# Kernel tuning notes

Hardware: AMD Instinct MI355X
Metric: run time of the kernel (lower is better)

Reference implementation:

```python
import jax, jax.numpy as jnp
import numpy as np

B, M, NH, EH = 16, 128, 256, 128


def setup_inputs() -> dict:
    key = jax.random.key(0)
    ks = jax.random.split(key, 10)
    s = 0.05
    return {
        "X": jax.random.normal(ks[0], (B, M, NH), dtype=jnp.float32),
        "E": jax.random.normal(ks[1], (B, M, M, EH), dtype=jnp.float32),
        "A": jax.random.uniform(ks[2], (B, M, M), dtype=jnp.float32),
        "w": jax.random.uniform(ks[3], (B, M, 1), dtype=jnp.float32),
        "Wv_w": jax.random.normal(ks[4], (NH, NH), dtype=jnp.float32) * s,
        "Wv_b": jnp.zeros((NH,), dtype=jnp.float32),
        "We_w": jax.random.normal(ks[5], (EH, EH), dtype=jnp.float32) * s,
        "We_b": jnp.zeros((EH,), dtype=jnp.float32),
        "Wu_w": jax.random.normal(ks[6], (2 * NH + EH, NH), dtype=jnp.float32) * s,
        "Wu_b": jnp.zeros((NH,), dtype=jnp.float32),
    }


def reference(X, E, A, w, Wv_w, Wv_b, We_w, We_b, Wu_w, Wu_b):
    act = jax.nn.relu
    # W_v / W_e single-layer FFNs (capacity=0 -> one Linear)
    node_map = X @ Wv_w + Wv_b                      # [B, m, nh]
    edge_map = E @ We_w + We_b                      # [B, m, m, eh]
    # Fused aggregation: sum_i A[b,i,j] * cat(node_map[b,i], edge_map[b,i,j])
    # (avoids materializing the [B,m,m,nh+eh] intermediate; same math)
    agg_node = jnp.einsum('bij,bid->bjd', A, node_map)   # [B, m, nh]
    agg_edge = jnp.einsum('bij,bije->bje', A, edge_map)  # [B, m, eh]
    h = jnp.concatenate([agg_node, agg_edge, X], axis=2) # [B, m, 2nh+eh]
    out = (act(h) @ Wu_w + Wu_b) * w                     # [B, m, nh]
    return out
```

## Files before the change

kernel.cpp:

```cpp
#include <hip/hip_runtime.h>

namespace {

constexpr int Bn   = 16;
constexpr int Mn   = 128;
constexpr int NHn  = 256;
constexpr int EHn  = 128;
constexpr int ROWS = Bn * Mn;
constexpr int HW   = 2 * NHn + EHn;

__device__ __forceinline__ float4 ld4(const float* p) {
    return *reinterpret_cast<const float4*>(p);
}
__device__ __forceinline__ float4 f4relu(const float4& a) {
    return make_float4(fmaxf(a.x, 0.f), fmaxf(a.y, 0.f),
                       fmaxf(a.z, 0.f), fmaxf(a.w, 0.f));
}

__global__ __launch_bounds__(256) void k_reduce(
    const float* __restrict__ E, const float* __restrict__ A,
    float* __restrict__ T)
{
    const int bid = blockIdx.x;
    const int b   = bid >> 5;
    const int j0  = (bid & 31) * 4;
    const int tid = threadIdx.x;

    __shared__ float acolT[4][Mn];

    if (tid < Mn) {
        const float4 a4 = ld4(A + (size_t)b * Mn * Mn + (size_t)tid * Mn + j0);
        acolT[0][tid] = a4.x; acolT[1][tid] = a4.y;
        acolT[2][tid] = a4.z; acolT[3][tid] = a4.w;
    }
    __syncthreads();

    const int jj = tid >> 6;
    const int f2 = tid & 63;
    const float* Eb = E + (size_t)b * Mn * Mn * EHn + (size_t)(j0 + jj) * EHn
                        + f2 * 2;
    const float* ac = acolT[jj];

    float2 acc = make_float2(0.f, 0.f);
    #pragma unroll 16
    for (int i = 0; i < Mn; ++i) {
        const float2 e2 = *reinterpret_cast<const float2*>(
            Eb + (size_t)i * (Mn * EHn));
        const float a = ac[i];
        acc.x = fmaf(a, e2.x, acc.x);
        acc.y = fmaf(a, e2.y, acc.y);
    }

    const int row = b * Mn + j0 + jj;
    *reinterpret_cast<float2*>(T + (size_t)row * EHn + f2 * 2) = acc;
}

__global__ __launch_bounds__(256) void k_mix(
    const float* __restrict__ T, const float* __restrict__ A,
    const float* __restrict__ X,
    const float* __restrict__ Wv, const float* __restrict__ Wvb,
    const float* __restrict__ We, const float* __restrict__ Web,
    const float* __restrict__ Wu, const float* __restrict__ Wub,
    const float* __restrict__ wrow, float* __restrict__ out)
{
    const int bid = blockIdx.x;
    const int b   = bid >> 5;
    const int j0  = (bid & 31) * 4;
    const int r0  = b * Mn + j0;
    const int tid = threadIdx.x;

    __shared__ float acolT[4][Mn];
    __shared__ float ts[4][EHn];
    __shared__ float axs[4][NHn];
    __shared__ float hs[4][HW];
    __shared__ float pec[2][4][EHn];
    __shared__ float pcs[4][16];
    __shared__ float csb[4];

    if (tid < Mn) {
        const float4 a4 = ld4(A + (size_t)b * Mn * Mn + (size_t)tid * Mn + j0);
        acolT[0][tid] = a4.x; acolT[1][tid] = a4.y;
        acolT[2][tid] = a4.z; acolT[3][tid] = a4.w;
    } else {
        const int t = tid - 128;
        const int r = t >> 5, c = t & 31;
        *reinterpret_cast<float4*>(&ts[r][c * 4]) =
            ld4(T + (size_t)(r0 + r) * EHn + c * 4);
    }
    {
        const int r = tid >> 6, c = tid & 63;
        const float4 x4 = ld4(X + (size_t)(r0 + r) * NHn + c * 4);
        *reinterpret_cast<float4*>(&hs[r][NHn + EHn + c * 4]) = f4relu(x4);
    }
    __syncthreads();

    if (tid < 64) {
        const int r = tid >> 4, s = tid & 15;
        float acc = 0.f;
        #pragma unroll
        for (int i = 0; i < 8; ++i) acc += acolT[r][s * 8 + i];
        pcs[r][s] = acc;
    }
    if (tid < 4) {
        float acc = 0.f;
        #pragma unroll
        for (int s = 0; s < 16; ++s) acc += pcs[tid][s];
        csb[tid] = acc;
    }

    {
        const float* Xb = X + (size_t)(b * Mn) * NHn + tid;
        float a0 = 0.f, a1 = 0.f, a2 = 0.f, a3 = 0.f;
        for (int k = 0; k < Mn; k += 16) {
            float xw[16];
            #pragma unroll
            for (int u = 0; u < 16; ++u) xw[u] = Xb[(size_t)(k + u) * NHn];
            #pragma unroll
            for (int u = 0; u < 16; ++u) {
                a0 = fmaf(acolT[0][k + u], xw[u], a0);
                a1 = fmaf(acolT[1][k + u], xw[u], a1);
                a2 = fmaf(acolT[2][k + u], xw[u], a2);
                a3 = fmaf(acolT[3][k + u], xw[u], a3);
            }
        }
        axs[0][tid] = a0; axs[1][tid] = a1;
        axs[2][tid] = a2; axs[3][tid] = a3;
    }
    __syncthreads();

    {
        const float* Wvc = Wv + tid;
        float n0 = 0.f, n1 = 0.f, n2 = 0.f, n3 = 0.f;
        for (int k = 0; k < NHn; k += 16) {
            float wv[16];
            #pragma unroll
            for (int u = 0; u < 16; ++u) wv[u] = Wvc[(size_t)(k + u) * NHn];
            #pragma unroll
            for (int u = 0; u < 16; ++u) {
                n0 = fmaf(axs[0][k + u], wv[u], n0);
                n1 = fmaf(axs[1][k + u], wv[u], n1);
                n2 = fmaf(axs[2][k + u], wv[u], n2);
                n3 = fmaf(axs[3][k + u], wv[u], n3);
            }
        }
        const float bv = Wvb[tid];
        hs[0][tid] = fmaxf(fmaf(csb[0], bv, n0), 0.f);
        hs[1][tid] = fmaxf(fmaf(csb[1], bv, n1), 0.f);
        hs[2][tid] = fmaxf(fmaf(csb[2], bv, n2), 0.f);
        hs[3][tid] = fmaxf(fmaf(csb[3], bv, n3), 0.f);
    }

    {
        const int kh = tid >> 7;
        const int c  = tid & 127;
        const int k0 = kh * 64;
        const float* Wec = We + c;
        float e0 = 0.f, e1 = 0.f, e2 = 0.f, e3 = 0.f;
        for (int k = k0; k < k0 + 64; k += 16) {
            float we[16];
            #pragma unroll
            for (int u = 0; u < 16; ++u) we[u] = Wec[(size_t)(k + u) * EHn];
            #pragma unroll
            for (int u = 0; u < 16; ++u) {
                e0 = fmaf(ts[0][k + u], we[u], e0);
                e1 = fmaf(ts[1][k + u], we[u], e1);
                e2 = fmaf(ts[2][k + u], we[u], e2);
                e3 = fmaf(ts[3][k + u], we[u], e3);
            }
        }
        pec[kh][0][c] = e0; pec[kh][1][c] = e1;
        pec[kh][2][c] = e2; pec[kh][3][c] = e3;
    }
    __syncthreads();
    if (tid < 128) {
        const float be = Web[tid];
        #pragma unroll
        for (int r = 0; r < 4; ++r) {
            const float e = pec[0][r][tid] + pec[1][r][tid];
            hs[r][NHn + tid] = fmaxf(fmaf(csb[r], be, e), 0.f);
        }
    }
    __syncthreads();

    {
        const float* Wuc = Wu + tid;
        float o0 = 0.f, o1 = 0.f, o2 = 0.f, o3 = 0.f;
        for (int k = 0; k < HW; k += 16) {
            float wu[16];
            #pragma unroll
            for (int u = 0; u < 16; ++u) wu[u] = Wuc[(size_t)(k + u) * NHn];
            #pragma unroll
            for (int u = 0; u < 16; ++u) {
                o0 = fmaf(hs[0][k + u], wu[u], o0);
                o1 = fmaf(hs[1][k + u], wu[u], o1);
                o2 = fmaf(hs[2][k + u], wu[u], o2);
                o3 = fmaf(hs[3][k + u], wu[u], o3);
            }
        }
        const float bu = Wub[tid];
        out[(size_t)(r0 + 0) * NHn + tid] = (o0 + bu) * wrow[r0 + 0];
        out[(size_t)(r0 + 1) * NHn + tid] = (o1 + bu) * wrow[r0 + 1];
        out[(size_t)(r0 + 2) * NHn + tid] = (o2 + bu) * wrow[r0 + 2];
        out[(size_t)(r0 + 3) * NHn + tid] = (o3 + bu) * wrow[r0 + 3];
    }
}

}

extern "C" void kernel_launch(void* const* d_in, const int* in_sizes, int n_in,
                              void* d_out, int out_size, void* d_ws, size_t ws_size,
                              hipStream_t stream) {
    const float* X   = (const float*)d_in[0];
    const float* E   = (const float*)d_in[1];
    const float* A   = (const float*)d_in[2];
    const float* w   = (const float*)d_in[3];
    const float* Wv  = (const float*)d_in[4];
    const float* Wvb = (const float*)d_in[5];
    const float* We  = (const float*)d_in[6];
    const float* Web = (const float*)d_in[7];
    const float* Wu  = (const float*)d_in[8];
    const float* Wub = (const float*)d_in[9];
    float* out = (float*)d_out;

    float* T = (float*)d_ws;

    k_reduce<<<512, 256, 0, stream>>>(E, A, T);
    k_mix<<<512, 256, 0, stream>>>(T, A, X, Wv, Wvb, We, Web, Wu, Wub, w, out);
}
```

Baseline: 258.8 us.

## Fuse edge reduction into mixing kernel and split i-range across thread halves

Merges the E·A reduction kernel into the mixing kernel, so the intermediate T buffer is never written to or read back from global memory and one launch is removed. Within the fused kernel, each thread reads float4 edge chunks and covers half of the i range, and the two partial sums are combined in shared memory. This adds an extra barrier and shared storage. Without a second kernel to overlap with, the memory-bound E stream now has to share each block with the matmul phases.

```diff
diff --git a/kernel.cpp b/kernel.cpp
--- a/kernel.cpp
+++ b/kernel.cpp
@@ -6,57 +6,24 @@
 constexpr int Mn   = 128;
 constexpr int NHn  = 256;
 constexpr int EHn  = 128;
-constexpr int ROWS = Bn * Mn;
 constexpr int HW   = 2 * NHn + EHn;
 
 __device__ __forceinline__ float4 ld4(const float* p) {
     return *reinterpret_cast<const float4*>(p);
+}
+__device__ __forceinline__ void f4fma(float4& acc, float a, const float4& v) {
+    acc.x = fmaf(a, v.x, acc.x);
+    acc.y = fmaf(a, v.y, acc.y);
+    acc.z = fmaf(a, v.z, acc.z);
+    acc.w = fmaf(a, v.w, acc.w);
 }
 __device__ __forceinline__ float4 f4relu(const float4& a) {
     return make_float4(fmaxf(a.x, 0.f), fmaxf(a.y, 0.f),
                        fmaxf(a.z, 0.f), fmaxf(a.w, 0.f));
 }
 
-__global__ __launch_bounds__(256) void k_reduce(
+__global__ __launch_bounds__(256) void k_fused(
     const float* __restrict__ E, const float* __restrict__ A,
-    float* __restrict__ T)
-{
-    const int bid = blockIdx.x;
-    const int b   = bid >> 5;
-    const int j0  = (bid & 31) * 4;
-    const int tid = threadIdx.x;
-
-    __shared__ float acolT[4][Mn];
-
-    if (tid < Mn) {
-        const float4 a4 = ld4(A + (size_t)b * Mn * Mn + (size_t)tid * Mn + j0);
-        acolT[0][tid] = a4.x; acolT[1][tid] = a4.y;
-        acolT[2][tid] = a4.z; acolT[3][tid] = a4.w;
-    }
-    __syncthreads();
-
-    const int jj = tid >> 6;
-    const int f2 = tid & 63;
-    const float* Eb = E + (size_t)b * Mn * Mn * EHn + (size_t)(j0 + jj) * EHn
-                        + f2 * 2;
-    const float* ac = acolT[jj];
-
-    float2 acc = make_float2(0.f, 0.f);
-    #pragma unroll 16
-    for (int i = 0; i < Mn; ++i) {
-        const float2 e2 = *reinterpret_cast<const float2*>(
-            Eb + (size_t)i * (Mn * EHn));
-        const float a = ac[i];
-        acc.x = fmaf(a, e2.x, acc.x);
-        acc.y = fmaf(a, e2.y, acc.y);
-    }
-
-    const int row = b * Mn + j0 + jj;
-    *reinterpret_cast<float2*>(T + (size_t)row * EHn + f2 * 2) = acc;
-}
-
-__global__ __launch_bounds__(256) void k_mix(
-    const float* __restrict__ T, const float* __restrict__ A,
     const float* __restrict__ X,
     const float* __restrict__ Wv, const float* __restrict__ Wvb,
     const float* __restrict__ We, const float* __restrict__ Web,
@@ -69,23 +36,19 @@
     const int r0  = b * Mn + j0;
     const int tid = threadIdx.x;
 
-    __shared__ float acolT[4][Mn];
-    __shared__ float ts[4][EHn];
-    __shared__ float axs[4][NHn];
-    __shared__ float hs[4][HW];
-    __shared__ float pec[2][4][EHn];
-    __shared__ float pcs[4][16];
-    __shared__ float csb[4];
+    __shared__ float  acolT[4][Mn];
+    __shared__ float4 pt[2][4][32];
+    __shared__ float  ts[4][EHn];
+    __shared__ float  axs[4][NHn];
+    __shared__ float  hs[4][HW];
+    __shared__ float  pec[2][4][EHn];
+    __shared__ float  pcs[4][16];
+    __shared__ float  csb[4];
 
     if (tid < Mn) {
         const float4 a4 = ld4(A + (size_t)b * Mn * Mn + (size_t)tid * Mn + j0);
         acolT[0][tid] = a4.x; acolT[1][tid] = a4.y;
         acolT[2][tid] = a4.z; acolT[3][tid] = a4.w;
-    } else {
-        const int t = tid - 128;
-        const int r = t >> 5, c = t & 31;
-        *reinterpret_cast<float4*>(&ts[r][c * 4]) =
-            ld4(T + (size_t)(r0 + r) * EHn + c * 4);
     }
     {
         const int r = tid >> 6, c = tid & 63;
@@ -109,6 +72,24 @@
     }
 
     {
+        const int ih = tid >> 7;
+        const int jj = (tid >> 5) & 3;
+        const int f4 = tid & 31;
+        const float* Eb = E + (size_t)b * Mn * Mn * EHn
+                            + (size_t)ih * (Mn * EHn)
+                            + (size_t)(j0 + jj) * EHn + f4 * 4;
+        const float* ac = acolT[jj];
+        float4 acc = make_float4(0.f, 0.f, 0.f, 0.f);
+        #pragma unroll 8
+        for (int it = 0; it < 64; ++it) {
+            const float a  = ac[2 * it + ih];
+            const float4 e4 = ld4(Eb + (size_t)it * (2 * Mn * EHn));
+            f4fma(acc, a, e4);
+        }
+        pt[ih][jj][f4] = acc;
+    }
+
+    {
         const float* Xb = X + (size_t)(b * Mn) * NHn + tid;
         float a0 = 0.f, a1 = 0.f, a2 = 0.f, a3 = 0.f;
         for (int k = 0; k < Mn; k += 16) {
@@ -127,6 +108,13 @@
         axs[2][tid] = a2; axs[3][tid] = a3;
     }
     __syncthreads();
+
+    if (tid < 128) {
+        const int jj = tid >> 5, f4 = tid & 31;
+        const float4 p0 = pt[0][jj][f4], p1 = pt[1][jj][f4];
+        *reinterpret_cast<float4*>(&ts[jj][f4 * 4]) =
+            make_float4(p0.x + p1.x, p0.y + p1.y, p0.z + p1.z, p0.w + p1.w);
+    }
 
     {
         const float* Wvc = Wv + tid;
@@ -149,6 +137,7 @@
         hs[2][tid] = fmaxf(fmaf(csb[2], bv, n2), 0.f);
         hs[3][tid] = fmaxf(fmaf(csb[3], bv, n3), 0.f);
     }
+    __syncthreads();
 
     {
         const int kh = tid >> 7;
@@ -222,8 +211,5 @@
     const float* Wub = (const float*)d_in[9];
     float* out = (float*)d_out;
 
-    float* T = (float*)d_ws;
-
-    k_reduce<<<512, 256, 0, stream>>>(E, A, T);
-    k_mix<<<512, 256, 0, stream>>>(T, A, X, Wv, Wvb, We, Web, Wu, Wub, w, out);
-}
+    k_fused<<<512, 256, 0, stream>>>(E, A, X, Wv, Wvb, We, Web, Wu, Wub, w, out);
+}
```

After: 253.9 us. Within noise of the previous version (-1.9%).
